# Kernel optimization log

Hardware: AMD Instinct MI355X
Metric: run time of the kernel (lower is better)

Reference implementation:

```python
import jax, jax.numpy as jnp
import numpy as np

B, H, W, C = 16, 32, 32, 512
L, CT = 77, 512
NH, HD = 8, 64
G = 32          # GroupNorm groups
EPS = 1e-6      # flax GroupNorm default epsilon
NEG = -1e10


def group_norm(x, scale, bias):
    # flax GroupNorm on [b, n, c]: stats over (n, channels-within-group) per (b, group)
    b, n, c = x.shape
    xg = x.reshape(b, n, G, c // G)
    mu = xg.mean(axis=(1, 3), keepdims=True)
    var = xg.var(axis=(1, 3), keepdims=True)
    xg = (xg - mu) * jax.lax.rsqrt(var + EPS)
    return xg.reshape(b, n, c) * scale + bias


def setup_inputs() -> dict:
    key = jax.random.key(0)
    ks = jax.random.split(key, 8)
    w = lambda k, shape: jax.random.normal(k, shape, jnp.float32) * 0.02
    return {
        "inputs": jax.random.normal(ks[0], (B, H, W, C), jnp.float32),
        "text_enc": jax.random.normal(ks[1], (B, L, CT), jnp.float32),
        "text_mask": jnp.ones((B, L), jnp.int32),
        "gn_q_scale": jnp.ones((C,), jnp.float32),
        "gn_q_bias": jnp.zeros((C,), jnp.float32),
        "gn_kv_scale": jnp.ones((C,), jnp.float32),
        "gn_kv_bias": jnp.zeros((C,), jnp.float32),
        "gn_t_scale": jnp.ones((CT,), jnp.float32),
        "gn_t_bias": jnp.zeros((CT,), jnp.float32),
        "Wq": w(ks[2], (C, NH, HD)),
        "Wk_self": w(ks[3], (C, NH, HD)),
        "Wv_self": w(ks[4], (C, NH, HD)),
        "Wk_cross": w(ks[5], (CT, NH, HD)),
        "Wv_cross": w(ks[6], (CT, NH, HD)),
        "Wout": w(ks[7], (NH, HD, C)),
    }


def reference(inputs, text_enc, text_mask,
              gn_q_scale, gn_q_bias, gn_kv_scale, gn_kv_bias,
              gn_t_scale, gn_t_bias,
              Wq, Wk_self, Wv_self, Wk_cross, Wv_cross, Wout):
    b, h, w, c = inputs.shape
    n = h * w
    x = inputs.reshape(b, n, c)

    x_q = group_norm(x, gn_q_scale, gn_q_bias)
    x_kv = group_norm(x, gn_kv_scale, gn_kv_bias)
    t = group_norm(text_enc, gn_t_scale, gn_t_bias)

    # q/k/v projections; fused: KV = concat(self-KV from image, cross-KV from text)
    scale = jnp.asarray(1.0 / np.sqrt(HD), inputs.dtype)
    q = jnp.einsum('bqc,chd->bqhd', x_q, Wq) * scale  # scale_attn_logits
    k = jnp.concatenate([jnp.einsum('bkc,chd->bkhd', x_kv, Wk_self),
                         jnp.einsum('blc,chd->blhd', t, Wk_cross)], axis=1)
    v = jnp.concatenate([jnp.einsum('bkc,chd->bkhd', x_kv, Wv_self),
                         jnp.einsum('blc,chd->blhd', t, Wv_cross)], axis=1)

    # make_attention_mask(ones[b,n], concat(ones[b,n], text_mask)) -> [b,1,n,n+l];
    # query mask is all ones so only the KV mask matters.
    kv_mask = jnp.concatenate(
        [jnp.ones((b, n), jnp.bool_), text_mask > 0], axis=1)  # [b, n+l]

    logits = jnp.einsum('bqhd,bkhd->bhqk', q, k)  # [b, nh, n, n+l]
    logits = jnp.where(kv_mask[:, None, None, :], logits, jnp.asarray(NEG, logits.dtype))
    probs = jax.nn.softmax(logits, axis=-1)
    attn = jnp.einsum('bhqk,bkhd->bqhd', probs, v)
    out = jnp.einsum('bqhd,hdc->bqc', attn, Wout)
    return out.reshape(b, h, w, c) + inputs
```

## Files before the change

### kernel.cpp

```cpp
#include <hip/hip_runtime.h>
#include <hip/hip_bf16.h>

typedef __hip_bfloat16 bf16;
typedef __attribute__((ext_vector_type(8))) short short8;
typedef __attribute__((ext_vector_type(4))) float f32x4;
typedef __attribute__((ext_vector_type(16))) float f32x16;
#define MFMA16(a, b, c) __builtin_amdgcn_mfma_f32_16x16x32_bf16(a, b, c, 0, 0, 0)
#define MFMA32(a, b, c) __builtin_amdgcn_mfma_f32_32x32x16_bf16(a, b, c, 0, 0, 0)

#define BB   16
#define CCH  512
#define NN   1024
#define LLT  77
#define LPAD 128
#define NHH  8
#define HDD  64
#define GGN  32
#define NKV  1101
#define KVP  1152

__device__ __forceinline__ unsigned short f2bu(float f){
  bf16 h = __float2bfloat16(f);
  return *reinterpret_cast<unsigned short*>(&h);
}

__device__ __forceinline__ unsigned pk2(float lo, float hi){
  __hip_bfloat162 h = __float22bfloat162_rn(make_float2(lo, hi));
  return *reinterpret_cast<unsigned*>(&h);
}

__device__ __forceinline__ void pl32swap(unsigned &a, unsigned &b){
  asm("v_permlane32_swap_b32 %0, %1" : "+v"(a), "+v"(b));
}

__global__ __launch_bounds__(256) void gn_stats_kernel(
    const float* __restrict__ ximg, const float* __restrict__ xtxt,
    float* __restrict__ stats )
{
  int isimg = blockIdx.x < 512;
  int bid = blockIdx.x & 511;
  int b = bid >> 5, g = bid & 31;
  int npos = isimg ? NN : LLT;
  const float* xb = (isimg ? ximg : xtxt) + (size_t)b * npos * CCH + g * 16;
  int tot4 = npos * 4;
  float s = 0.f, s2 = 0.f;
  for (int e = threadIdx.x; e < tot4; e += 256){
    int n = e >> 2, cq = (e & 3) * 4;
    float4 v = *(const float4*)(xb + (size_t)n * CCH + cq);
    s  += v.x + v.y + v.z + v.w;
    s2 += v.x * v.x + v.y * v.y + v.z * v.z + v.w * v.w;
  }
  __shared__ float sh1[256], sh2[256];
  sh1[threadIdx.x] = s; sh2[threadIdx.x] = s2;
  __syncthreads();
  for (int off = 128; off > 0; off >>= 1){
    if (threadIdx.x < off){
      sh1[threadIdx.x] += sh1[threadIdx.x + off];
      sh2[threadIdx.x] += sh2[threadIdx.x + off];
    }
    __syncthreads();
  }
  if (threadIdx.x == 0){
    float inv = 1.f / (float)(npos * 16);
    float m = sh1[0] * inv;
    float var = sh2[0] * inv - m * m;
    float* mu = stats + (isimg ? 0 : 1024);
    mu[bid] = m;
    mu[512 + bid] = rsqrtf(var + 1e-6f);
  }
}

__global__ __launch_bounds__(256) void prep_weights_kernel(
    const float* __restrict__ W0, const float* __restrict__ W1,
    const float* __restrict__ W2, const float* __restrict__ W3,
    const float* __restrict__ W4, const float* __restrict__ W5,
    bf16* __restrict__ Wt)
{
  int wsel = blockIdx.z;
  const float* W = wsel == 0 ? W0 : wsel == 1 ? W1 : wsel == 2 ? W2 :
                   wsel == 3 ? W3 : wsel == 4 ? W4 : W5;
  bf16* dst = Wt + (size_t)wsel * CCH * CCH;
  int n0 = blockIdx.x * 64, k0 = blockIdx.y * 64;

  __shared__ alignas(16) float Ws[64][68];
  int r = threadIdx.x >> 2, c = (threadIdx.x & 3) * 16;
  const float* src = W + (size_t)(k0 + r) * CCH + n0 + c;
  *(float4*)&Ws[r][c]      = *(const float4*)(src);
  *(float4*)&Ws[r][c + 4]  = *(const float4*)(src + 4);
  *(float4*)&Ws[r][c + 8]  = *(const float4*)(src + 8);
  *(float4*)&Ws[r][c + 12] = *(const float4*)(src + 12);
  __syncthreads();

  int nr = threadIdx.x >> 2, kc = (threadIdx.x & 3) * 16;
  union { uint4 v[2]; unsigned short s[16]; } o;
  #pragma unroll
  for (int j = 0; j < 16; j++) o.s[j] = f2bu(Ws[kc + j][nr]);
  bf16* d = dst + (size_t)(n0 + nr) * CCH + k0 + kc;
  *(uint4*)d = o.v[0];
  *(uint4*)(d + 8) = o.v[1];
}

__global__ __launch_bounds__(256) void norm_all_kernel(
    const float* __restrict__ x, const float* __restrict__ t,
    const float* __restrict__ stats,
    const float* __restrict__ gqs, const float* __restrict__ gqb,
    const float* __restrict__ gks, const float* __restrict__ gkb,
    const float* __restrict__ gts, const float* __restrict__ gtb,
    bf16* __restrict__ Xq, bf16* __restrict__ Xkv, bf16* __restrict__ Tn)
{
  if (blockIdx.x < 4096){
    size_t e = ((size_t)blockIdx.x * 256 + threadIdx.x) * 8;
    int b  = (int)(e >> 19);
    int ch = (int)(e & 511);
    int g  = ch >> 4;
    float m = stats[b * GGN + g], r = stats[512 + b * GGN + g];
    float4 x0 = *(const float4*)(x + e);
    float4 x1 = *(const float4*)(x + e + 4);
    float4 sq0 = *(const float4*)(gqs + ch), sq1 = *(const float4*)(gqs + ch + 4);
    float4 bq0 = *(const float4*)(gqb + ch), bq1 = *(const float4*)(gqb + ch + 4);
    float4 sk0 = *(const float4*)(gks + ch), sk1 = *(const float4*)(gks + ch + 4);
    float4 bk0 = *(const float4*)(gkb + ch), bk1 = *(const float4*)(gkb + ch + 4);
    float xs[8] = {x0.x,x0.y,x0.z,x0.w,x1.x,x1.y,x1.z,x1.w};
    float sqv[8] = {sq0.x,sq0.y,sq0.z,sq0.w,sq1.x,sq1.y,sq1.z,sq1.w};
    float bqv[8] = {bq0.x,bq0.y,bq0.z,bq0.w,bq1.x,bq1.y,bq1.z,bq1.w};
    float skv[8] = {sk0.x,sk0.y,sk0.z,sk0.w,sk1.x,sk1.y,sk1.z,sk1.w};
    float bkv[8] = {bk0.x,bk0.y,bk0.z,bk0.w,bk1.x,bk1.y,bk1.z,bk1.w};
    union { uint4 v; unsigned short s[8]; } oq, ok;
    #pragma unroll
    for (int j = 0; j < 8; j++){
      float nx = (xs[j] - m) * r;
      oq.s[j] = f2bu((nx * sqv[j] + bqv[j]) * 0.18033688f);
      ok.s[j] = f2bu(nx * skv[j] + bkv[j]);
    }
    *(uint4*)(Xq + e)  = oq.v;
    *(uint4*)(Xkv + e) = ok.v;
  } else {
    size_t e = ((size_t)(blockIdx.x - 4096) * 256 + threadIdx.x) * 8;
    int b  = (int)(e >> 16);
    int rem = (int)(e & 65535);
    int l  = rem >> 9;
    int ch = rem & 511;
    union { uint4 v; unsigned short s[8]; } o;
    if (l < LLT){
      int g = ch >> 4;
      float m = stats[1024 + b * GGN + g], r = stats[1536 + b * GGN + g];
      const float* src = t + ((size_t)b * LLT + l) * CCH + ch;
      float4 x0 = *(const float4*)src, x1 = *(const float4*)(src + 4);
      float4 s0 = *(const float4*)(gts + ch), s1 = *(const float4*)(gts + ch + 4);
      float4 b0 = *(const float4*)(gtb + ch), b1 = *(const float4*)(gtb + ch + 4);
      float xs[8] = {x0.x,x0.y,x0.z,x0.w,x1.x,x1.y,x1.z,x1.w};
      float sv[8] = {s0.x,s0.y,s0.z,s0.w,s1.x,s1.y,s1.z,s1.w};
      float bv[8] = {b0.x,b0.y,b0.z,b0.w,b1.x,b1.y,b1.z,b1.w};
      #pragma unroll
      for (int j = 0; j < 8; j++) o.s[j] = f2bu((xs[j] - m) * r * sv[j] + bv[j]);
    } else {
      o.v = make_uint4(0, 0, 0, 0);
    }
    *(uint4*)(Tn + e) = o.v;
  }
}

__global__ __launch_bounds__(256) void proj_self_mfma(
    const bf16* __restrict__ Xq, const bf16* __restrict__ Xkv,
    const bf16* __restrict__ Wt,
    bf16* __restrict__ Qo, bf16* __restrict__ Ko, bf16* __restrict__ Vo)
{
  const int tid  = threadIdx.x;
  const int wave = tid >> 6, lane = tid & 63;
  const int l16 = lane & 15, quad = lane >> 4;
  const int wr = wave >> 1, wc = wave & 1;
  const int ct = blockIdx.x;
  const int rt = blockIdx.y;
  const int mat = ct >> 2;
  const int cm0 = (ct & 3) * 128;
  const int b  = rt >> 3;
  const int n0 = (rt & 7) * 128;

  __shared__ bf16 T[4][64][72];

  const bf16* A  = (mat == 0) ? Xq : Xkv;
  const bf16* Bw = Wt + (size_t)mat * CCH * CCH + (size_t)cm0 * CCH;

  f32x4 acc[4][4];
  #pragma unroll
  for (int rf = 0; rf < 4; rf++)
    #pragma unroll
    for (int cf = 0; cf < 4; cf++) acc[rf][cf] = (f32x4){0.f,0.f,0.f,0.f};

  const int sr = tid >> 2, sc = (tid & 3) * 16;
  const bf16* pa0 = A  + ((size_t)b * NN + n0 + sr) * CCH + sc;
  const bf16* pa1 = pa0 + (size_t)64 * CCH;
  const bf16* pb0 = Bw + (size_t)sr * CCH + sc;
  const bf16* pb1 = pb0 + (size_t)64 * CCH;

  uint4 rA0a = *(const uint4*)pa0, rA0b = *(const uint4*)(pa0 + 8);
  uint4 rA1a = *(const uint4*)pa1, rA1b = *(const uint4*)(pa1 + 8);
  uint4 rB0a = *(const uint4*)pb0, rB0b = *(const uint4*)(pb0 + 8);
  uint4 rB1a = *(const uint4*)pb1, rB1b = *(const uint4*)(pb1 + 8);

  for (int kt = 0; kt < 8; kt++){
    *(uint4*)&T[0][sr][sc] = rA0a;  *(uint4*)&T[0][sr][sc + 8] = rA0b;
    *(uint4*)&T[1][sr][sc] = rA1a;  *(uint4*)&T[1][sr][sc + 8] = rA1b;
    *(uint4*)&T[2][sr][sc] = rB0a;  *(uint4*)&T[2][sr][sc + 8] = rB0b;
    *(uint4*)&T[3][sr][sc] = rB1a;  *(uint4*)&T[3][sr][sc + 8] = rB1b;
    if (kt < 7){
      const int k1 = (kt + 1) * 64;
      rA0a = *(const uint4*)(pa0 + k1);  rA0b = *(const uint4*)(pa0 + k1 + 8);
      rA1a = *(const uint4*)(pa1 + k1);  rA1b = *(const uint4*)(pa1 + k1 + 8);
      rB0a = *(const uint4*)(pb0 + k1);  rB0b = *(const uint4*)(pb0 + k1 + 8);
      rB1a = *(const uint4*)(pb1 + k1);  rB1b = *(const uint4*)(pb1 + k1 + 8);
    }
    __syncthreads();

    short8 af[4][2];
    #pragma unroll
    for (int rf = 0; rf < 4; rf++){
      af[rf][0] = *(const short8*)&T[wr][rf * 16 + l16][quad * 8];
      af[rf][1] = *(const short8*)&T[wr][rf * 16 + l16][32 + quad * 8];
    }
    #pragma unroll
    for (int cf = 0; cf < 4; cf++){
      const short8 b0 = *(const short8*)&T[2 + wc][cf * 16 + l16][quad * 8];
      const short8 b1 = *(const short8*)&T[2 + wc][cf * 16 + l16][32 + quad * 8];
      #pragma unroll
      for (int rf = 0; rf < 4; rf++){
        acc[rf][cf] = MFMA16(af[rf][0], b0, acc[rf][cf]);
        acc[rf][cf] = MFMA16(af[rf][1], b1, acc[rf][cf]);
      }
    }
    __syncthreads();
  }

  if (mat < 2){
    bf16* Out = (mat == 0) ? Qo : Ko;
    const int stride = (mat == 0) ? NN : KVP;
    #pragma unroll
    for (int cf = 0; cf < 4; cf++){
      const int cm = cm0 + wc * 64 + cf * 16 + l16;
      const int h = cm >> 6, d = cm & 63;
      #pragma unroll
      for (int rf = 0; rf < 4; rf++)
        #pragma unroll
        for (int r = 0; r < 4; r++){
          const int n = n0 + wr * 64 + rf * 16 + quad * 4 + r;
          Out[(((size_t)b * NHH + h) * stride + n) * HDD + d] =
              __float2bfloat16(acc[rf][cf][r]);
        }
    }
  } else {
    bf16 (*Tw)[72] = T[wave];
    #pragma unroll
    for (int cf = 0; cf < 4; cf++)
      #pragma unroll
      for (int rf = 0; rf < 4; rf++)
        #pragma unroll
        for (int r = 0; r < 4; r++)
          Tw[cf * 16 + l16][rf * 16 + quad * 4 + r] =
              __float2bfloat16(acc[rf][cf][r]);
    __syncthreads();
    const int h  = (cm0 + wc * 64) >> 6;
    const int nb = n0 + wr * 64;
    const int dl = lane >> 2, cseg = (lane & 3) * 16;
    #pragma unroll
    for (int k2 = 0; k2 < 4; k2++){
      const int d = dl + k2 * 16;
      bf16* vd = Vo + (((size_t)b * NHH + h) * HDD + d) * KVP + nb + cseg;
      *(uint4*)vd       = *(const uint4*)&Tw[d][cseg];
      *(uint4*)(vd + 8) = *(const uint4*)&Tw[d][cseg + 8];
    }
  }
}

__global__ __launch_bounds__(256) void proj_cross_mfma(
    const bf16* __restrict__ Tn, const bf16* __restrict__ Wt,
    bf16* __restrict__ Ko, bf16* __restrict__ Vo)
{
  const int tid  = threadIdx.x;
  const int wave = tid >> 6, lane = tid & 63;
  const int l16 = lane & 15, quad = lane >> 4;
  const int h  = blockIdx.x;
  const int l0 = blockIdx.y * 64;
  const int b  = blockIdx.z;

  __shared__ bf16 At[64][72];
  __shared__ bf16 Bk[64][72], Bv[64][72];

  const bf16* Wkc = Wt + 3 * CCH * CCH;
  const bf16* Wvc = Wt + 4 * CCH * CCH;

  f32x4 sk[4], sv[4];
  #pragma unroll
  for (int nt = 0; nt < 4; nt++){
    sk[nt] = (f32x4){0.f,0.f,0.f,0.f};
    sv[nt] = (f32x4){0.f,0.f,0.f,0.f};
  }

  const int sr = tid >> 2, sc = (tid & 3) * 16;
  const bf16* p_a  = Tn  + ((size_t)b * LPAD + l0 + sr) * CCH + sc;
  const bf16* p_bk = Wkc + (size_t)(h * 64 + sr) * CCH + sc;
  const bf16* p_bv = Wvc + (size_t)(h * 64 + sr) * CCH + sc;

  uint4 ra0 = *(const uint4*)p_a,   ra1 = *(const uint4*)(p_a + 8);
  uint4 rk0 = *(const uint4*)p_bk,  rk1 = *(const uint4*)(p_bk + 8);
  uint4 rv0 = *(const uint4*)p_bv,  rv1 = *(const uint4*)(p_bv + 8);

  for (int kt = 0; kt < 8; kt++){
    *(uint4*)&At[sr][sc]     = ra0;  *(uint4*)&At[sr][sc + 8] = ra1;
    *(uint4*)&Bk[sr][sc]     = rk0;  *(uint4*)&Bk[sr][sc + 8] = rk1;
    *(uint4*)&Bv[sr][sc]     = rv0;  *(uint4*)&Bv[sr][sc + 8] = rv1;
    if (kt < 7){
      const int k1 = (kt + 1) * 64;
      ra0 = *(const uint4*)(p_a + k1);   ra1 = *(const uint4*)(p_a + k1 + 8);
      rk0 = *(const uint4*)(p_bk + k1);  rk1 = *(const uint4*)(p_bk + k1 + 8);
      rv0 = *(const uint4*)(p_bv + k1);  rv1 = *(const uint4*)(p_bv + k1 + 8);
    }
    __syncthreads();

    const short8 a0 = *(const short8*)&At[wave * 16 + l16][quad * 8];
    const short8 a1 = *(const short8*)&At[wave * 16 + l16][32 + quad * 8];
    #pragma unroll
    for (int nt = 0; nt < 4; nt++){
      const short8 bk0 = *(const short8*)&Bk[nt * 16 + l16][quad * 8];
      const short8 bk1 = *(const short8*)&Bk[nt * 16 + l16][32 + quad * 8];
      sk[nt] = MFMA16(a0, bk0, sk[nt]);
      sk[nt] = MFMA16(a1, bk1, sk[nt]);
      const short8 bv0 = *(const short8*)&Bv[nt * 16 + l16][quad * 8];
      const short8 bv1 = *(const short8*)&Bv[nt * 16 + l16][32 + quad * 8];
      sv[nt] = MFMA16(a0, bv0, sv[nt]);
      sv[nt] = MFMA16(a1, bv1, sv[nt]);
    }
    __syncthreads();
  }

  #pragma unroll
  for (int r = 0; r < 4; r++){
    int kvrow = NN + l0 + wave * 16 + quad * 4 + r;
    bf16* kd = Ko + (((size_t)b * NHH + h) * KVP + kvrow) * HDD + l16;
    #pragma unroll
    for (int nt = 0; nt < 4; nt++)
      kd[nt * 16] = __float2bfloat16(sk[nt][r]);
  }

  __syncthreads();
  #pragma unroll
  for (int nt = 0; nt < 4; nt++)
    #pragma unroll
    for (int r = 0; r < 4; r++)
      Bk[nt * 16 + l16][wave * 16 + quad * 4 + r] = __float2bfloat16(sv[nt][r]);
  __syncthreads();
  {
    int d = tid >> 2, c = (tid & 3) * 16;
    bf16* vd = Vo + (((size_t)b * NHH + h) * HDD + d) * KVP + NN + l0 + c;
    *(uint4*)vd       = *(const uint4*)&Bk[d][c];
    *(uint4*)(vd + 8) = *(const uint4*)&Bk[d][c + 8];
  }
}

__global__ __launch_bounds__(256, 4) void attn_mfma_kernel(
    const bf16* __restrict__ Q, const bf16* __restrict__ K,
    const bf16* __restrict__ Vt, const int* __restrict__ tmask,
    bf16* __restrict__ Ao)
{
  const int tid  = threadIdx.x;
  const int wave = tid >> 6;
  const int lane = tid & 63;
  const int l31  = lane & 31;
  const int hi   = lane >> 5;
  const int q0 = blockIdx.x * 128;
  const int h  = blockIdx.y;
  const int b  = blockIdx.z;

  __shared__ alignas(16) bf16 KV[2][2][64][72];

  const bf16* qp = Q + (((size_t)b * NHH + h) * NN + q0 + wave * 32 + l31) * HDD + hi * 8;
  short8 qf[4];
  qf[0] = *(const short8*)(qp);
  qf[1] = *(const short8*)(qp + 16);
  qf[2] = *(const short8*)(qp + 32);
  qf[3] = *(const short8*)(qp + 48);

  union { unsigned u[4]; short8 s8; } ones;
  ones.u[0] = 0x3F803F80u; ones.u[1] = 0x3F803F80u;
  ones.u[2] = 0x3F803F80u; ones.u[3] = 0x3F803F80u;

  f32x16 zf;
  #pragma unroll
  for (int i = 0; i < 16; i++) zf[i] = 0.f;

  f32x16 o_acc[2], l_acc;
  #pragma unroll
  for (int dt = 0; dt < 2; dt++)
    #pragma unroll
    for (int i = 0; i < 16; i++) o_acc[dt][i] = 0.f;
  #pragma unroll
  for (int i = 0; i < 16; i++) l_acc[i] = 0.f;

  const size_t kbase = ((size_t)b * NHH + h) * KVP;
  const size_t vbase = ((size_t)b * NHH + h) * (size_t)HDD * KVP;

  const int sr = tid >> 2;
  const int sc = (tid & 3) * 16;
  const bf16* kp = K  + (kbase + sr) * HDD + sc;
  const bf16* vp = Vt + vbase + (size_t)sr * KVP + sc;

  uint4 kr0 = *(const uint4*)kp, kr1 = *(const uint4*)(kp + 8);
  uint4 vr0 = *(const uint4*)vp, vr1 = *(const uint4*)(vp + 8);
  *(uint4*)&KV[0][0][sr][sc]     = kr0;
  *(uint4*)&KV[0][0][sr][sc + 8] = kr1;
  *(uint4*)&KV[0][1][sr][sc]     = vr0;
  *(uint4*)&KV[0][1][sr][sc + 8] = vr1;
  kr0 = *(const uint4*)(kp + 4096); kr1 = *(const uint4*)(kp + 4096 + 8);
  vr0 = *(const uint4*)(vp + 64);   vr1 = *(const uint4*)(vp + 64 + 8);
  __syncthreads();

  for (int kt = 0; kt < 18; kt++){
    const int cur = kt & 1;
    if (kt + 1 < 18){
      *(uint4*)&KV[cur ^ 1][0][sr][sc]     = kr0;
      *(uint4*)&KV[cur ^ 1][0][sr][sc + 8] = kr1;
      *(uint4*)&KV[cur ^ 1][1][sr][sc]     = vr0;
      *(uint4*)&KV[cur ^ 1][1][sr][sc + 8] = vr1;
    }
    if (kt + 2 < 18){
      const size_t ko = (size_t)(kt + 2) * 4096;
      const int    vo = (kt + 2) * 64;
      kr0 = *(const uint4*)(kp + ko); kr1 = *(const uint4*)(kp + ko + 8);
      vr0 = *(const uint4*)(vp + vo); vr1 = *(const uint4*)(vp + vo + 8);
    }

    const bf16 (*Ks)[72] = KV[cur][0];
    const bf16 (*Vs)[72] = KV[cur][1];
    const int kv0 = kt * 64;

    #pragma unroll
    for (int t = 0; t < 2; t++){
      const short8 kf0 = *(const short8*)&Ks[t * 32 + l31][hi * 8];
      const short8 kf1 = *(const short8*)&Ks[t * 32 + l31][16 + hi * 8];
      const short8 kf2 = *(const short8*)&Ks[t * 32 + l31][32 + hi * 8];
      const short8 kf3 = *(const short8*)&Ks[t * 32 + l31][48 + hi * 8];
      f32x16 s = MFMA32(kf0, qf[0], zf);
      s = MFMA32(kf1, qf[1], s);
      s = MFMA32(kf2, qf[2], s);
      s = MFMA32(kf3, qf[3], s);

      if (kv0 + 64 > NN){
        #pragma unroll
        for (int r = 0; r < 16; r++){
          int idx = kv0 - NN + t * 32 + (r & 3) + 8 * (r >> 2) + 4 * hi;
          int ci = idx < LLT ? idx : LLT - 1;
          float rep = (idx < LLT)
                        ? (tmask[b * LLT + ci] > 0 ? 1e30f : -1e10f)
                        : -1e30f;
          s[r] = fminf(s[r], rep);
        }
      }

      #pragma unroll
      for (int r = 0; r < 16; r++) s[r] = exp2f(s[r]);

      unsigned w0 = pk2(s[0],  s[1]),  w1 = pk2(s[2],  s[3]);
      unsigned w2 = pk2(s[4],  s[5]),  w3 = pk2(s[6],  s[7]);
      unsigned w4 = pk2(s[8],  s[9]),  w5 = pk2(s[10], s[11]);
      unsigned w6 = pk2(s[12], s[13]), w7 = pk2(s[14], s[15]);
      pl32swap(w0, w2);
      pl32swap(w1, w3);
      pl32swap(w4, w6);
      pl32swap(w5, w7);
      union { unsigned u[4]; short8 s8; } pf0, pf1;
      pf0.u[0] = w0; pf0.u[1] = w1; pf0.u[2] = w2; pf0.u[3] = w3;
      pf1.u[0] = w4; pf1.u[1] = w5; pf1.u[2] = w6; pf1.u[3] = w7;

      l_acc = MFMA32(pf0.s8, ones.s8, l_acc);
      l_acc = MFMA32(pf1.s8, ones.s8, l_acc);

      #pragma unroll
      for (int dt = 0; dt < 2; dt++){
        const short8 vf0 = *(const short8*)&Vs[dt * 32 + l31][t * 32 + hi * 8];
        const short8 vf1 = *(const short8*)&Vs[dt * 32 + l31][t * 32 + 16 + hi * 8];
        o_acc[dt] = MFMA32(pf0.s8, vf0, o_acc[dt]);
        o_acc[dt] = MFMA32(pf1.s8, vf1, o_acc[dt]);
      }
    }
    __syncthreads();
  }

  #pragma unroll
  for (int r = 0; r < 16; r++){
    const int ql = (r & 3) + 8 * (r >> 2) + 4 * hi;
    const float linv = 1.f / l_acc[r];
    const int n = q0 + wave * 32 + ql;
    bf16* dst = Ao + ((size_t)b * NN + n) * CCH + h * HDD + l31;
    dst[0]  = __float2bfloat16(o_acc[0][r] * linv);
    dst[32] = __float2bfloat16(o_acc[1][r] * linv);
  }
}

__global__ __launch_bounds__(256) void outproj_mfma(
    const bf16* __restrict__ A, const bf16* __restrict__ Wt,
    const float* __restrict__ resid, float* __restrict__ out)
{
  const int tid  = threadIdx.x;
  const int wave = tid >> 6, lane = tid & 63;
  const int l16 = lane & 15, quad = lane >> 4;
  const int wr = wave >> 1, wc = wave & 1;
  const int c0 = blockIdx.x * 128;
  const int g0 = blockIdx.y * 128;

  __shared__ bf16 T[4][64][72];
  const bf16* Bw = Wt + (size_t)5 * CCH * CCH + (size_t)c0 * CCH;

  f32x4 acc[4][4];
  #pragma unroll
  for (int rf = 0; rf < 4; rf++)
    #pragma unroll
    for (int cf = 0; cf < 4; cf++) acc[rf][cf] = (f32x4){0.f,0.f,0.f,0.f};

  const int sr = tid >> 2, sc = (tid & 3) * 16;
  const bf16* pa0 = A  + ((size_t)g0 + sr) * CCH + sc;
  const bf16* pa1 = pa0 + (size_t)64 * CCH;
  const bf16* pb0 = Bw + (size_t)sr * CCH + sc;
  const bf16* pb1 = pb0 + (size_t)64 * CCH;

  uint4 rA0a = *(const uint4*)pa0, rA0b = *(const uint4*)(pa0 + 8);
  uint4 rA1a = *(const uint4*)pa1, rA1b = *(const uint4*)(pa1 + 8);
  uint4 rB0a = *(const uint4*)pb0, rB0b = *(const uint4*)(pb0 + 8);
  uint4 rB1a = *(const uint4*)pb1, rB1b = *(const uint4*)(pb1 + 8);

  for (int kt = 0; kt < 8; kt++){
    *(uint4*)&T[0][sr][sc] = rA0a;  *(uint4*)&T[0][sr][sc + 8] = rA0b;
    *(uint4*)&T[1][sr][sc] = rA1a;  *(uint4*)&T[1][sr][sc + 8] = rA1b;
    *(uint4*)&T[2][sr][sc] = rB0a;  *(uint4*)&T[2][sr][sc + 8] = rB0b;
    *(uint4*)&T[3][sr][sc] = rB1a;  *(uint4*)&T[3][sr][sc + 8] = rB1b;
    if (kt < 7){
      const int k1 = (kt + 1) * 64;
      rA0a = *(const uint4*)(pa0 + k1);  rA0b = *(const uint4*)(pa0 + k1 + 8);
      rA1a = *(const uint4*)(pa1 + k1);  rA1b = *(const uint4*)(pa1 + k1 + 8);
      rB0a = *(const uint4*)(pb0 + k1);  rB0b = *(const uint4*)(pb0 + k1 + 8);
      rB1a = *(const uint4*)(pb1 + k1);  rB1b = *(const uint4*)(pb1 + k1 + 8);
    }
    __syncthreads();

    short8 af[4][2];
    #pragma unroll
    for (int rf = 0; rf < 4; rf++){
      af[rf][0] = *(const short8*)&T[wr][rf * 16 + l16][quad * 8];
      af[rf][1] = *(const short8*)&T[wr][rf * 16 + l16][32 + quad * 8];
    }
    #pragma unroll
    for (int cf = 0; cf < 4; cf++){
      const short8 b0 = *(const short8*)&T[2 + wc][cf * 16 + l16][quad * 8];
      const short8 b1 = *(const short8*)&T[2 + wc][cf * 16 + l16][32 + quad * 8];
      #pragma unroll
      for (int rf = 0; rf < 4; rf++){
        acc[rf][cf] = MFMA16(af[rf][0], b0, acc[rf][cf]);
        acc[rf][cf] = MFMA16(af[rf][1], b1, acc[rf][cf]);
      }
    }
    __syncthreads();
  }

  #pragma unroll
  for (int rf = 0; rf < 4; rf++)
    #pragma unroll
    for (int r = 0; r < 4; r++){
      const size_t row = (size_t)g0 + wr * 64 + rf * 16 + quad * 4 + r;
      #pragma unroll
      for (int cf = 0; cf < 4; cf++){
        const int col = c0 + wc * 64 + cf * 16 + l16;
        out[row * CCH + col] = acc[rf][cf][r] + resid[row * CCH + col];
      }
    }
}

extern "C" void kernel_launch(void* const* d_in, const int* in_sizes, int n_in,
                              void* d_out, int out_size, void* d_ws, size_t ws_size,
                              hipStream_t stream)
{
  const float* x     = (const float*)d_in[0];
  const float* txt   = (const float*)d_in[1];
  const int*   tmask = (const int*)d_in[2];
  const float* gqs   = (const float*)d_in[3];
  const float* gqb   = (const float*)d_in[4];
  const float* gks   = (const float*)d_in[5];
  const float* gkb   = (const float*)d_in[6];
  const float* gts   = (const float*)d_in[7];
  const float* gtb   = (const float*)d_in[8];
  const float* Wq    = (const float*)d_in[9];
  const float* Wks   = (const float*)d_in[10];
  const float* Wvs   = (const float*)d_in[11];
  const float* Wkc   = (const float*)d_in[12];
  const float* Wvc   = (const float*)d_in[13];
  const float* Wout  = (const float*)d_in[14];

  float* stats = (float*)d_ws;
  bf16* WtAll = (bf16*)(stats + 2048);
  bf16* Xq  = WtAll + (size_t)6 * CCH * CCH;
  bf16* Xkv = Xq  + (size_t)BB * NN * CCH;
  bf16* Tn  = Xkv + (size_t)BB * NN * CCH;
  bf16* Qw  = Tn  + (size_t)BB * LPAD * CCH;
  bf16* Kw  = Qw  + (size_t)BB * NHH * NN * HDD;
  bf16* Vw  = Kw  + (size_t)BB * NHH * KVP * HDD;
  bf16* Aw  = Xq;

  gn_stats_kernel<<<1024, 256, 0, stream>>>(x, txt, stats);
  prep_weights_kernel<<<dim3(8, 8, 6), 256, 0, stream>>>(
      Wq, Wks, Wvs, Wkc, Wvc, Wout, WtAll);
  norm_all_kernel<<<4608, 256, 0, stream>>>(
      x, txt, stats, gqs, gqb, gks, gkb, gts, gtb, Xq, Xkv, Tn);
  proj_self_mfma<<<dim3(12, 128), 256, 0, stream>>>(
      Xq, Xkv, WtAll, Qw, Kw, Vw);
  proj_cross_mfma<<<dim3(8, 2, BB), 256, 0, stream>>>(
      Tn, WtAll, Kw, Vw);
  attn_mfma_kernel<<<dim3(8, NHH, BB), 256, 0, stream>>>(Qw, Kw, Vw, tmask, Aw);
  outproj_mfma<<<dim3(4, 128), 256, 0, stream>>>(Aw, WtAll, x, (float*)d_out);
}
```

Before: 277.7 us.

## Use native bf16 pack/exp asm, flatten grids, add MFMA setprio and hoist V loads

Replaces the bf16 conversion helpers with packed v_cvt_pk_bf16_f32 and exp2f with raw v_exp_f32 in the attention softmax. Flattens the 2D/3D grids to 1D so that consecutive blocks share weight columns or K/V heads, aiming at better cache reuse. Adds s_setprio around the MFMA groups and hoists the V fragment loads ahead of the PV MFMAs to improve overlap. The raw exp instruction drops the denormal and range handling that exp2f does, and the new block order changes which blocks run at the same time.

```diff
diff --git a/kernel.cpp b/kernel.cpp
--- a/kernel.cpp
+++ b/kernel.cpp
@@ -25,8 +25,15 @@
 }
 
 __device__ __forceinline__ unsigned pk2(float lo, float hi){
-  __hip_bfloat162 h = __float22bfloat162_rn(make_float2(lo, hi));
-  return *reinterpret_cast<unsigned*>(&h);
+  unsigned r;
+  asm("v_cvt_pk_bf16_f32 %0, %1, %2" : "=v"(r) : "v"(lo), "v"(hi));
+  return r;
+}
+
+__device__ __forceinline__ float fexp2(float x){
+  float r;
+  asm("v_exp_f32 %0, %1" : "=v"(r) : "v"(x));
+  return r;
 }
 
 __device__ __forceinline__ void pl32swap(unsigned &a, unsigned &b){
@@ -92,12 +99,18 @@
   __syncthreads();
 
   int nr = threadIdx.x >> 2, kc = (threadIdx.x & 3) * 16;
-  union { uint4 v[2]; unsigned short s[16]; } o;
-  #pragma unroll
-  for (int j = 0; j < 16; j++) o.s[j] = f2bu(Ws[kc + j][nr]);
+  uint4 o0, o1;
+  o0.x = pk2(Ws[kc + 0][nr],  Ws[kc + 1][nr]);
+  o0.y = pk2(Ws[kc + 2][nr],  Ws[kc + 3][nr]);
+  o0.z = pk2(Ws[kc + 4][nr],  Ws[kc + 5][nr]);
+  o0.w = pk2(Ws[kc + 6][nr],  Ws[kc + 7][nr]);
+  o1.x = pk2(Ws[kc + 8][nr],  Ws[kc + 9][nr]);
+  o1.y = pk2(Ws[kc + 10][nr], Ws[kc + 11][nr]);
+  o1.z = pk2(Ws[kc + 12][nr], Ws[kc + 13][nr]);
+  o1.w = pk2(Ws[kc + 14][nr], Ws[kc + 15][nr]);
   bf16* d = dst + (size_t)(n0 + nr) * CCH + k0 + kc;
-  *(uint4*)d = o.v[0];
-  *(uint4*)(d + 8) = o.v[1];
+  *(uint4*)d = o0;
+  *(uint4*)(d + 8) = o1;
 }
 
 __global__ __launch_bounds__(256) void norm_all_kernel(
@@ -125,22 +138,27 @@
     float bqv[8] = {bq0.x,bq0.y,bq0.z,bq0.w,bq1.x,bq1.y,bq1.z,bq1.w};
     float skv[8] = {sk0.x,sk0.y,sk0.z,sk0.w,sk1.x,sk1.y,sk1.z,sk1.w};
     float bkv[8] = {bk0.x,bk0.y,bk0.z,bk0.w,bk1.x,bk1.y,bk1.z,bk1.w};
-    union { uint4 v; unsigned short s[8]; } oq, ok;
+    float q[8], k[8];
     #pragma unroll
     for (int j = 0; j < 8; j++){
       float nx = (xs[j] - m) * r;
-      oq.s[j] = f2bu((nx * sqv[j] + bqv[j]) * 0.18033688f);
-      ok.s[j] = f2bu(nx * skv[j] + bkv[j]);
-    }
-    *(uint4*)(Xq + e)  = oq.v;
-    *(uint4*)(Xkv + e) = ok.v;
+      q[j] = (nx * sqv[j] + bqv[j]) * 0.18033688f;
+      k[j] = nx * skv[j] + bkv[j];
+    }
+    uint4 oq, ok;
+    oq.x = pk2(q[0], q[1]); oq.y = pk2(q[2], q[3]);
+    oq.z = pk2(q[4], q[5]); oq.w = pk2(q[6], q[7]);
+    ok.x = pk2(k[0], k[1]); ok.y = pk2(k[2], k[3]);
+    ok.z = pk2(k[4], k[5]); ok.w = pk2(k[6], k[7]);
+    *(uint4*)(Xq + e)  = oq;
+    *(uint4*)(Xkv + e) = ok;
   } else {
     size_t e = ((size_t)(blockIdx.x - 4096) * 256 + threadIdx.x) * 8;
     int b  = (int)(e >> 16);
     int rem = (int)(e & 65535);
     int l  = rem >> 9;
     int ch = rem & 511;
-    union { uint4 v; unsigned short s[8]; } o;
+    uint4 o;
     if (l < LLT){
       int g = ch >> 4;
       float m = stats[1024 + b * GGN + g], r = stats[1536 + b * GGN + g];
@@ -151,12 +169,15 @@
       float xs[8] = {x0.x,x0.y,x0.z,x0.w,x1.x,x1.y,x1.z,x1.w};
       float sv[8] = {s0.x,s0.y,s0.z,s0.w,s1.x,s1.y,s1.z,s1.w};
       float bv[8] = {b0.x,b0.y,b0.z,b0.w,b1.x,b1.y,b1.z,b1.w};
+      float w[8];
       #pragma unroll
-      for (int j = 0; j < 8; j++) o.s[j] = f2bu((xs[j] - m) * r * sv[j] + bv[j]);
+      for (int j = 0; j < 8; j++) w[j] = (xs[j] - m) * r * sv[j] + bv[j];
+      o.x = pk2(w[0], w[1]); o.y = pk2(w[2], w[3]);
+      o.z = pk2(w[4], w[5]); o.w = pk2(w[6], w[7]);
     } else {
-      o.v = make_uint4(0, 0, 0, 0);
-    }
-    *(uint4*)(Tn + e) = o.v;
+      o = make_uint4(0, 0, 0, 0);
+    }
+    *(uint4*)(Tn + e) = o;
   }
 }
 
@@ -169,8 +190,9 @@
   const int wave = tid >> 6, lane = tid & 63;
   const int l16 = lane & 15, quad = lane >> 4;
   const int wr = wave >> 1, wc = wave & 1;
-  const int ct = blockIdx.x;
-  const int rt = blockIdx.y;
+  const int bx = blockIdx.x;
+  const int ct = bx >> 7;
+  const int rt = bx & 127;
   const int mat = ct >> 2;
   const int cm0 = (ct & 3) * 128;
   const int b  = rt >> 3;
@@ -366,9 +388,11 @@
   const int lane = tid & 63;
   const int l31  = lane & 31;
   const int hi   = lane >> 5;
-  const int q0 = blockIdx.x * 128;
-  const int h  = blockIdx.y;
-  const int b  = blockIdx.z;
+  const int bx = blockIdx.x;
+  const int q0 = (bx >> 7) * 128;
+  const int g  = bx & 127;
+  const int h  = g & 7;
+  const int b  = g >> 3;
 
   __shared__ alignas(16) bf16 KV[2][2][64][72];
 
@@ -438,10 +462,12 @@
       const short8 kf1 = *(const short8*)&Ks[t * 32 + l31][16 + hi * 8];
       const short8 kf2 = *(const short8*)&Ks[t * 32 + l31][32 + hi * 8];
       const short8 kf3 = *(const short8*)&Ks[t * 32 + l31][48 + hi * 8];
+      __builtin_amdgcn_s_setprio(1);
       f32x16 s = MFMA32(kf0, qf[0], zf);
       s = MFMA32(kf1, qf[1], s);
       s = MFMA32(kf2, qf[2], s);
       s = MFMA32(kf3, qf[3], s);
+      __builtin_amdgcn_s_setprio(0);
 
       if (kv0 + 64 > NN){
         #pragma unroll
@@ -456,7 +482,7 @@
       }
 
       #pragma unroll
-      for (int r = 0; r < 16; r++) s[r] = exp2f(s[r]);
+      for (int r = 0; r < 16; r++) s[r] = fexp2(s[r]);
 
       unsigned w0 = pk2(s[0],  s[1]),  w1 = pk2(s[2],  s[3]);
       unsigned w2 = pk2(s[4],  s[5]),  w3 = pk2(s[6],  s[7]);
@@ -470,16 +496,19 @@
       pf0.u[0] = w0; pf0.u[1] = w1; pf0.u[2] = w2; pf0.u[3] = w3;
       pf1.u[0] = w4; pf1.u[1] = w5; pf1.u[2] = w6; pf1.u[3] = w7;
 
+      const short8 vf00 = *(const short8*)&Vs[l31][t * 32 + hi * 8];
+      const short8 vf01 = *(const short8*)&Vs[l31][t * 32 + 16 + hi * 8];
+      const short8 vf10 = *(const short8*)&Vs[32 + l31][t * 32 + hi * 8];
+      const short8 vf11 = *(const short8*)&Vs[32 + l31][t * 32 + 16 + hi * 8];
+
+      __builtin_amdgcn_s_setprio(1);
       l_acc = MFMA32(pf0.s8, ones.s8, l_acc);
       l_acc = MFMA32(pf1.s8, ones.s8, l_acc);
-
-      #pragma unroll
-      for (int dt = 0; dt < 2; dt++){
-        const short8 vf0 = *(const short8*)&Vs[dt * 32 + l31][t * 32 + hi * 8];
-        const short8 vf1 = *(const short8*)&Vs[dt * 32 + l31][t * 32 + 16 + hi * 8];
-        o_acc[dt] = MFMA32(pf0.s8, vf0, o_acc[dt]);
-        o_acc[dt] = MFMA32(pf1.s8, vf1, o_acc[dt]);
-      }
+      o_acc[0] = MFMA32(pf0.s8, vf00, o_acc[0]);
+      o_acc[0] = MFMA32(pf1.s8, vf01, o_acc[0]);
+      o_acc[1] = MFMA32(pf0.s8, vf10, o_acc[1]);
+      o_acc[1] = MFMA32(pf1.s8, vf11, o_acc[1]);
+      __builtin_amdgcn_s_setprio(0);
     }
     __syncthreads();
   }
@@ -503,8 +532,9 @@
   const int wave = tid >> 6, lane = tid & 63;
   const int l16 = lane & 15, quad = lane >> 4;
   const int wr = wave >> 1, wc = wave & 1;
-  const int c0 = blockIdx.x * 128;
-  const int g0 = blockIdx.y * 128;
+  const int bx = blockIdx.x;
+  const int c0 = (bx >> 7) * 128;
+  const int g0 = (bx & 127) * 128;
 
   __shared__ bf16 T[4][64][72];
   const bf16* Bw = Wt + (size_t)5 * CCH * CCH + (size_t)c0 * CCH;
@@ -607,10 +637,10 @@
       Wq, Wks, Wvs, Wkc, Wvc, Wout, WtAll);
   norm_all_kernel<<<4608, 256, 0, stream>>>(
       x, txt, stats, gqs, gqb, gks, gkb, gts, gtb, Xq, Xkv, Tn);
-  proj_self_mfma<<<dim3(12, 128), 256, 0, stream>>>(
+  proj_self_mfma<<<1536, 256, 0, stream>>>(
       Xq, Xkv, WtAll, Qw, Kw, Vw);
   proj_cross_mfma<<<dim3(8, 2, BB), 256, 0, stream>>>(
       Tn, WtAll, Kw, Vw);
-  attn_mfma_kernel<<<dim3(8, NHH, BB), 256, 0, stream>>>(Qw, Kw, Vw, tmask, Aw);
-  outproj_mfma<<<dim3(4, 128), 256, 0, stream>>>(Aw, WtAll, x, (float*)d_out);
-}
+  attn_mfma_kernel<<<1024, 256, 0, stream>>>(Qw, Kw, Vw, tmask, Aw);
+  outproj_mfma<<<512, 256, 0, stream>>>(Aw, WtAll, x, (float*)d_out);
+}
```

Measured after the change: 251.4 us. 1.1x faster.
